# Kernel optimization log

Hardware: AMD Instinct MI355X
Metric: run time of the kernel (lower is better)

The kernel has to match this reference:

```python
import jax, jax.numpy as jnp
import numpy as np

SURROGATE_SCALE = 10.0  # SuperSpike-style surrogate slope

@jax.custom_vjp
def spike_fn(v):
    # Heaviside step: spike if membrane minus threshold > 0
    return (v > 0).astype(v.dtype)

def _spike_fwd(v):
    return spike_fn(v), v

def _spike_bwd(v, g):
    # SuperSpike surrogate gradient: 1 / (scale*|v| + 1)^2
    sg = 1.0 / jnp.square(SURROGATE_SCALE * jnp.abs(v) + 1.0)
    return (g * sg,)

spike_fn.defvjp(_spike_fwd, _spike_bwd)


def setup_inputs() -> dict:
    key = jax.random.key(0)
    B, C, T = 64, 256, 2000
    x = jax.random.normal(key, (B, C, T), dtype=jnp.float32)
    alpha = jnp.float32(0.75)
    beta = jnp.float32(0.65)
    Vth = jnp.ones((C,), dtype=jnp.float32)
    return {"x": x, "alpha": alpha, "beta": beta, "Vth": Vth}


def reference(x, alpha, beta, Vth):
    # LIF membrane recurrence over time (neuron_type='LIF', flatten_output=False)
    # x: (B, C, T) -> spk_rec: (B, C, T)
    B, C, T = x.shape
    xs = jnp.transpose(x, (2, 0, 1))  # (T, B, C)

    def step(carry, x_t):
        mem, spk = carry
        rst = spk * Vth                      # einsum('ab,b->ab', spk, Vth)
        mem = (mem - rst) * beta + x_t * alpha  # LIF scales input by alpha
        spk = spike_fn(mem - Vth)
        return (mem, spk), spk

    init = (jnp.zeros((B, C), x.dtype), jnp.zeros((B, C), x.dtype))
    _, spk_rec = jax.lax.scan(step, init, xs)  # (T, B, C)
    return jnp.transpose(spk_rec, (1, 2, 0))   # (B, C, T)
```

## Files before the change

### kernel.cpp

```cpp
#include <hip/hip_runtime.h>


constexpr int T_LEN = 2000;
constexpr int NV    = 10;
constexpr int CH    = NV * 4;
constexpr int NC    = T_LEN / CH;

__device__ __forceinline__ void load_chunk(float4 (&buf)[NV], const float4* __restrict__ xr, int c) {
#pragma unroll
    for (int v = 0; v < NV; ++v) buf[v] = xr[c * NV + v];
}

__device__ __forceinline__ float lif_step(float xval, float alpha, float beta, float vth,
                                          float& mem, float& vdiff, bool& spk) {
#pragma clang fp contract(off)
    float xa = xval * alpha;
    float p0 = mem   * beta;
    float p1 = vdiff * beta;
    float q0 = p0 + xa;
    float q1 = p1 + xa;
    mem   = spk ? q1 : q0;
    vdiff = mem - vth;
    spk   = vdiff > 0.0f;
    return spk ? 1.0f : 0.0f;
}

__device__ __forceinline__ void compute_chunk(const float4 (&buf)[NV], float4* __restrict__ orow, int c,
                                              float alpha, float beta, float vth,
                                              float& mem, float& vdiff, bool& spk) {
#pragma clang fp contract(off)
#pragma unroll
    for (int v = 0; v < NV; ++v) {
        float4 xv = buf[v];
        float4 s;
        s.x = lif_step(xv.x, alpha, beta, vth, mem, vdiff, spk);
        s.y = lif_step(xv.y, alpha, beta, vth, mem, vdiff, spk);
        s.z = lif_step(xv.z, alpha, beta, vth, mem, vdiff, spk);
        s.w = lif_step(xv.w, alpha, beta, vth, mem, vdiff, spk);
        orow[c * NV + v] = s;
    }
}

__global__ __launch_bounds__(64) void lif_fwd_kernel(const float* __restrict__ x,
                                                     const float* __restrict__ alpha_p,
                                                     const float* __restrict__ beta_p,
                                                     const float* __restrict__ vth_p,
                                                     float* __restrict__ out,
                                                     int C, int rows) {
#pragma clang fp contract(off)
    const int row = blockIdx.x * 64 + threadIdx.x;
    if (row >= rows) return;

    const float alpha = alpha_p[0];
    const float beta  = beta_p[0];
    const float vth   = vth_p[(unsigned)row % (unsigned)C];

    const float4* __restrict__ xr   = reinterpret_cast<const float4*>(x + (size_t)row * T_LEN);
    float4* __restrict__       orow = reinterpret_cast<float4*>(out + (size_t)row * T_LEN);

    float mem = 0.0f, vdiff = 0.0f;
    bool  spk = false;

    float4 A[NV], B[NV];
    load_chunk(A, xr, 0);

    for (int i = 0; i < NC / 2; ++i) {
        const int c = 2 * i;
        load_chunk(B, xr, c + 1);
        compute_chunk(A, orow, c, alpha, beta, vth, mem, vdiff, spk);
        if (c + 2 < NC) load_chunk(A, xr, c + 2);
        compute_chunk(B, orow, c + 1, alpha, beta, vth, mem, vdiff, spk);
    }
}

extern "C" void kernel_launch(void* const* d_in, const int* in_sizes, int n_in,
                              void* d_out, int out_size, void* d_ws, size_t ws_size,
                              hipStream_t stream) {
    const float* x     = (const float*)d_in[0];
    const float* alpha = (const float*)d_in[1];
    const float* beta  = (const float*)d_in[2];
    const float* vth   = (const float*)d_in[3];
    float* out = (float*)d_out;

    const int C    = in_sizes[3];
    const int rows = in_sizes[0] / T_LEN;

    dim3 grid((rows + 63) / 64), block(64);
    lif_fwd_kernel<<<grid, block, 0, stream>>>(x, alpha, beta, vth, out, C, rows);
}
```

Baseline: 259.4 us.

## Triple-buffer input chunks with inline-asm loads and explicit vmcnt waits

Measured after the change: 255.5 us. No clear change (-1.5%).

```diff
diff --git a/kernel.cpp b/kernel.cpp
--- a/kernel.cpp
+++ b/kernel.cpp
@@ -6,10 +6,21 @@
 constexpr int CH    = NV * 4;
 constexpr int NC    = T_LEN / CH;
 
-__device__ __forceinline__ void load_chunk(float4 (&buf)[NV], const float4* __restrict__ xr, int c) {
-#pragma unroll
-    for (int v = 0; v < NV; ++v) buf[v] = xr[c * NV + v];
-}
+typedef float nfloat4 __attribute__((ext_vector_type(4)));
+
+#define GL(dst, p, OFF) \
+    asm volatile("global_load_dwordx4 %0, %1, off offset:" #OFF \
+                 : "=v"(dst) : "v"(p))
+
+#define LOAD_CHUNK(buf, p) do { \
+    GL(buf[0], (p), 0);   GL(buf[1], (p), 16);  GL(buf[2], (p), 32); \
+    GL(buf[3], (p), 48);  GL(buf[4], (p), 64);  GL(buf[5], (p), 80); \
+    GL(buf[6], (p), 96);  GL(buf[7], (p), 112); GL(buf[8], (p), 128); \
+    GL(buf[9], (p), 144); } while (0)
+
+#define WAITV(N) do { \
+    asm volatile("s_waitcnt vmcnt(" #N ")" ::: "memory"); \
+    __builtin_amdgcn_sched_barrier(0); } while (0)
 
 __device__ __forceinline__ float lif_step(float xval, float alpha, float beta, float vth,
                                           float& mem, float& vdiff, bool& spk) {
@@ -25,13 +36,13 @@
     return spk ? 1.0f : 0.0f;
 }
 
-__device__ __forceinline__ void compute_chunk(const float4 (&buf)[NV], float4* __restrict__ orow, int c,
+__device__ __forceinline__ void compute_chunk(const nfloat4 (&buf)[NV], float4* __restrict__ orow, int c,
                                               float alpha, float beta, float vth,
                                               float& mem, float& vdiff, bool& spk) {
 #pragma clang fp contract(off)
 #pragma unroll
     for (int v = 0; v < NV; ++v) {
-        float4 xv = buf[v];
+        nfloat4 xv = buf[v];
         float4 s;
         s.x = lif_step(xv.x, alpha, beta, vth, mem, vdiff, spk);
         s.y = lif_step(xv.y, alpha, beta, vth, mem, vdiff, spk);
@@ -55,22 +66,51 @@
     const float beta  = beta_p[0];
     const float vth   = vth_p[(unsigned)row % (unsigned)C];
 
+    asm volatile("" :: "v"(alpha), "v"(beta), "v"(vth));
+
     const float4* __restrict__ xr   = reinterpret_cast<const float4*>(x + (size_t)row * T_LEN);
     float4* __restrict__       orow = reinterpret_cast<float4*>(out + (size_t)row * T_LEN);
 
     float mem = 0.0f, vdiff = 0.0f;
     bool  spk = false;
 
-    float4 A[NV], B[NV];
-    load_chunk(A, xr, 0);
+    nfloat4 A[NV], B[NV], Cb[NV];
 
-    for (int i = 0; i < NC / 2; ++i) {
-        const int c = 2 * i;
-        load_chunk(B, xr, c + 1);
+    LOAD_CHUNK(A, xr);
+    LOAD_CHUNK(B, xr + NV);
+
+    LOAD_CHUNK(Cb, xr + 2 * NV);
+    WAITV(20);
+    compute_chunk(A, orow, 0, alpha, beta, vth, mem, vdiff, spk);
+
+    LOAD_CHUNK(A, xr + 3 * NV);
+    WAITV(30);
+    compute_chunk(B, orow, 1, alpha, beta, vth, mem, vdiff, spk);
+
+    LOAD_CHUNK(B, xr + 4 * NV);
+    WAITV(40);
+    compute_chunk(Cb, orow, 2, alpha, beta, vth, mem, vdiff, spk);
+
+    int c = 3;
+    for (int i = 0; i < 15; ++i) {
+        LOAD_CHUNK(Cb, xr + (c + 2) * NV);
+        WAITV(40);
         compute_chunk(A, orow, c, alpha, beta, vth, mem, vdiff, spk);
-        if (c + 2 < NC) load_chunk(A, xr, c + 2);
+
+        LOAD_CHUNK(A, xr + (c + 3) * NV);
+        WAITV(40);
         compute_chunk(B, orow, c + 1, alpha, beta, vth, mem, vdiff, spk);
+
+        LOAD_CHUNK(B, xr + (c + 4) * NV);
+        WAITV(40);
+        compute_chunk(Cb, orow, c + 2, alpha, beta, vth, mem, vdiff, spk);
+
+        c += 3;
     }
+    WAITV(30);
+    compute_chunk(A, orow, 48, alpha, beta, vth, mem, vdiff, spk);
+    WAITV(20);
+    compute_chunk(B, orow, 49, alpha, beta, vth, mem, vdiff, spk);
 }
 
 extern "C" void kernel_launch(void* const* d_in, const int* in_sizes, int n_in,
```

## Stage spike outputs through LDS to coalesce global stores across rows

Applied to the files above, without the earlier changes.

After: 250.1 us. 3.6% less time.

```diff
diff --git a/kernel.cpp b/kernel.cpp
--- a/kernel.cpp
+++ b/kernel.cpp
@@ -2,13 +2,20 @@
 
 
 constexpr int T_LEN = 2000;
-constexpr int NV    = 10;
-constexpr int CH    = NV * 4;
-constexpr int NC    = T_LEN / CH;
+constexpr int CH    = 32;
+constexpr int NQ    = CH / 4;
+constexpr int NFULL = 62;
+constexpr int TAILQ = (T_LEN - NFULL * CH)/4;
+constexpr int LDSW  = 33;
 
-__device__ __forceinline__ void load_chunk(float4 (&buf)[NV], const float4* __restrict__ xr, int c) {
+__device__ __forceinline__ void load_tile(float4 (&buf)[NQ], const float4* __restrict__ p) {
 #pragma unroll
-    for (int v = 0; v < NV; ++v) buf[v] = xr[c * NV + v];
+    for (int q = 0; q < NQ; ++q) buf[q] = p[q];
+}
+
+__device__ __forceinline__ void load_tail(float4 (&buf)[NQ], const float4* __restrict__ p) {
+#pragma unroll
+    for (int q = 0; q < TAILQ; ++q) buf[q] = p[q];
 }
 
 __device__ __forceinline__ float lif_step(float xval, float alpha, float beta, float vth,
@@ -25,19 +32,28 @@
     return spk ? 1.0f : 0.0f;
 }
 
-__device__ __forceinline__ void compute_chunk(const float4 (&buf)[NV], float4* __restrict__ orow, int c,
-                                              float alpha, float beta, float vth,
-                                              float& mem, float& vdiff, bool& spk) {
+template <int N>
+__device__ __forceinline__ void compute_tile(const float4 (&buf)[NQ], float* shrow,
+                                             float alpha, float beta, float vth,
+                                             float& mem, float& vdiff, bool& spk) {
 #pragma clang fp contract(off)
 #pragma unroll
-    for (int v = 0; v < NV; ++v) {
-        float4 xv = buf[v];
-        float4 s;
-        s.x = lif_step(xv.x, alpha, beta, vth, mem, vdiff, spk);
-        s.y = lif_step(xv.y, alpha, beta, vth, mem, vdiff, spk);
-        s.z = lif_step(xv.z, alpha, beta, vth, mem, vdiff, spk);
-        s.w = lif_step(xv.w, alpha, beta, vth, mem, vdiff, spk);
-        orow[c * NV + v] = s;
+    for (int q = 0; q < N; ++q) {
+        float4 xv = buf[q];
+        shrow[q*4 + 0] = lif_step(xv.x, alpha, beta, vth, mem, vdiff, spk);
+        shrow[q*4 + 1] = lif_step(xv.y, alpha, beta, vth, mem, vdiff, spk);
+        shrow[q*4 + 2] = lif_step(xv.z, alpha, beta, vth, mem, vdiff, spk);
+        shrow[q*4 + 3] = lif_step(xv.w, alpha, beta, vth, mem, vdiff, spk);
+    }
+}
+
+__device__ __forceinline__ void store_tile(const float* __restrict__ sh, int sub, int off,
+                                           float* __restrict__ op) {
+#pragma unroll
+    for (int k = 0; k < 8; ++k) {
+        const float* p = sh + (sub + 8*k) * LDSW + off * 4;
+        float4 s = make_float4(p[0], p[1], p[2], p[3]);
+        *reinterpret_cast<float4*>(op + (size_t)(8*k) * T_LEN) = s;
     }
 }
 
@@ -48,28 +64,62 @@
                                                      float* __restrict__ out,
                                                      int C, int rows) {
 #pragma clang fp contract(off)
-    const int row = blockIdx.x * 64 + threadIdx.x;
+    __shared__ float sh[64 * LDSW];
+
+    const int lane = threadIdx.x;
+    const int row0 = blockIdx.x * 64;
+    const int row  = row0 + lane;
     if (row >= rows) return;
 
     const float alpha = alpha_p[0];
     const float beta  = beta_p[0];
     const float vth   = vth_p[(unsigned)row % (unsigned)C];
 
-    const float4* __restrict__ xr   = reinterpret_cast<const float4*>(x + (size_t)row * T_LEN);
-    float4* __restrict__       orow = reinterpret_cast<float4*>(out + (size_t)row * T_LEN);
+    const float4* __restrict__ xq = reinterpret_cast<const float4*>(x + (size_t)row * T_LEN);
+    float* __restrict__ shrow = sh + lane * LDSW;
+    const int sub = lane >> 3;
+    const int off = lane & 7;
+    float* __restrict__ outp = out + (size_t)(row0 + sub) * T_LEN + off * 4;
 
     float mem = 0.0f, vdiff = 0.0f;
     bool  spk = false;
+    float4 A[NQ], B[NQ];
 
-    float4 A[NV], B[NV];
-    load_chunk(A, xr, 0);
+    load_tile(A, xq);
+    int t = 0;
+    for (int i = 0; i < 30; ++i) {
+        load_tile(B, xq + (size_t)(t + 1) * NQ);
+        __builtin_amdgcn_sched_barrier(0);
+        compute_tile<NQ>(A, shrow, alpha, beta, vth, mem, vdiff, spk);
+        store_tile(sh, sub, off, outp + (size_t)t * CH);
+        ++t;
+        load_tile(A, xq + (size_t)(t + 1) * NQ);
+        __builtin_amdgcn_sched_barrier(0);
+        compute_tile<NQ>(B, shrow, alpha, beta, vth, mem, vdiff, spk);
+        store_tile(sh, sub, off, outp + (size_t)t * CH);
+        ++t;
+    }
+    load_tile(B, xq + (size_t)61 * NQ);
+    __builtin_amdgcn_sched_barrier(0);
+    compute_tile<NQ>(A, shrow, alpha, beta, vth, mem, vdiff, spk);
+    store_tile(sh, sub, off, outp + (size_t)60 * CH);
 
-    for (int i = 0; i < NC / 2; ++i) {
-        const int c = 2 * i;
-        load_chunk(B, xr, c + 1);
-        compute_chunk(A, orow, c, alpha, beta, vth, mem, vdiff, spk);
-        if (c + 2 < NC) load_chunk(A, xr, c + 2);
-        compute_chunk(B, orow, c + 1, alpha, beta, vth, mem, vdiff, spk);
+    load_tail(A, xq + (size_t)62 * NQ);
+    __builtin_amdgcn_sched_barrier(0);
+    compute_tile<NQ>(B, shrow, alpha, beta, vth, mem, vdiff, spk);
+    store_tile(sh, sub, off, outp + (size_t)61 * CH);
+
+    compute_tile<TAILQ>(A, shrow, alpha, beta, vth, mem, vdiff, spk);
+    {
+        const int subt = lane >> 2;
+        const int offt = lane & 3;
+        float* opt = out + (size_t)(row0 + subt) * T_LEN + NFULL * CH + offt * 4;
+#pragma unroll
+        for (int k = 0; k < 4; ++k) {
+            const float* p = sh + (subt + 16*k) * LDSW + offt * 4;
+            float4 s = make_float4(p[0], p[1], p[2], p[3]);
+            *reinterpret_cast<float4*>(opt + (size_t)(16*k) * T_LEN) = s;
+        }
     }
 }
 
```
